# Kernel optimization log

Hardware: AMD Instinct MI355X
Metric: run time of the kernel (lower is better)

Reference implementation:

```python
import jax, jax.numpy as jnp
import numpy as np

N, K = 16384, 16          # nodes, neighbors per node
IN, HID, OUT = 256, 512, 512
HEADS, A = 8, 64          # heads * attention_size = 512
EPS = 1e-5


def _layernorm(x, g, b):
    m = x.mean(-1, keepdims=True)
    v = x.var(-1, keepdims=True)
    return (x - m) / jnp.sqrt(v + EPS) * g + b


def setup_inputs() -> dict:
    key = jax.random.key(0)
    ks = jax.random.split(key, 16)
    def lin(k, i, o):
        kw, kb = jax.random.split(k)
        w = jax.random.normal(kw, (i, o), jnp.float32) / np.sqrt(i).astype(np.float32)
        b = jax.random.normal(kb, (o,), jnp.float32) * 0.01
        return w, b
    inp = {}
    inp["data"] = jax.random.normal(ks[0], (N, IN), jnp.float32)
    inp["neighbors"] = jax.random.randint(ks[1], (N, K), 0, N, jnp.int32)
    inp["mlp_w0"], inp["mlp_b0"] = lin(ks[2], IN, HID)
    inp["mlp_w1"], inp["mlp_b1"] = lin(ks[3], HID, HID)
    inp["mlp_w2"], inp["mlp_b2"] = lin(ks[4], HID, HID)
    inp["pd_w"], inp["pd_b"] = lin(ks[5], IN, HID)   # project_down
    inp["pi_w"], inp["pi_b"] = lin(ks[6], IN, OUT)   # project_in
    inp["q_w"], inp["q_b"] = lin(ks[7], HID, HEADS * A)
    inp["k_w"], inp["k_b"] = lin(ks[8], HID, HEADS * A)
    inp["v_w"], inp["v_b"] = lin(ks[9], HID, HEADS * A)
    inp["o_w"], inp["o_b"] = lin(ks[10], HEADS * A, OUT)
    inp["ln1_g"] = jnp.ones((HID,), jnp.float32)
    inp["ln1_b"] = jnp.zeros((HID,), jnp.float32)
    inp["ln2_g"] = jnp.ones((OUT,), jnp.float32)
    inp["ln2_b"] = jnp.zeros((OUT,), jnp.float32)
    return inp


def reference(data, neighbors, mlp_w0, mlp_b0, mlp_w1, mlp_b1, mlp_w2, mlp_b2,
              pd_w, pd_b, pi_w, pi_b, q_w, q_b, k_w, k_b, v_w, v_b, o_w, o_b,
              ln1_g, ln1_b, ln2_g, ln2_b):
    # --- local MLP branch (3-layer MLP, elu between layers) ---
    h = jax.nn.elu(data @ mlp_w0 + mlp_b0)
    h = jax.nn.elu(h @ mlp_w1 + mlp_b1)
    h = h @ mlp_w2 + mlp_b2
    pd = data @ pd_w + pd_b                 # project_down(data), reused twice
    local = h + pd                          # MLP(data) + project_down(data)
    # dropout is identity in eval mode
    local = jax.nn.elu(_layernorm(local + pd, ln1_g, ln1_b))
    # --- neighbour dot multi-head attention ---
    q = (local @ q_w + q_b).reshape(N, HEADS, A)
    kk = (local @ k_w + k_b)
    vv = (local @ v_w + v_b)
    kn = kk[neighbors].reshape(N, K, HEADS, A)   # irregular gather
    vn = vv[neighbors].reshape(N, K, HEADS, A)
    scores = jnp.einsum('nha,nkha->nhk', q, kn) / np.float32(np.sqrt(A))
    w = jax.nn.softmax(scores, axis=-1)
    attn = jnp.einsum('nhk,nkha->nha', w, vn).reshape(N, HEADS * A)
    interaction = attn @ o_w + o_b
    # --- residual + output norm ---
    return _layernorm(interaction + data @ pi_w + pi_b, ln2_g, ln2_b)
```

## Files before the change

### kernel.cpp

```cpp
#include <hip/hip_runtime.h>
#include <hip/hip_fp8.h>

typedef _Float16 h16;
typedef _Float16 h16x8 __attribute__((ext_vector_type(8)));
typedef _Float16 h16x4 __attribute__((ext_vector_type(4)));
typedef _Float16 h16x2 __attribute__((ext_vector_type(2)));
typedef float f32x4 __attribute__((ext_vector_type(4)));

#define DEV static __device__ __forceinline__

static constexpr size_t OFF_DATA = 0;
static constexpr size_t OFF_W0T  = 4194304;
static constexpr size_t OFF_W1T  = 4325376;
static constexpr size_t OFF_W2PD = 4587520;
static constexpr size_t OFF_QKVT = 4980736;
static constexpr size_t OFF_OPIT = 5767168;
static constexpr size_t OFF_X1   = 6160384;
static constexpr size_t OFF_X2   = 14548992;
static constexpr size_t OFF_P    = 22937600;

DEV void gload16(const void* g, void* l)
{
    __builtin_amdgcn_global_load_lds(
        (__attribute__((address_space(1))) void*)(void*)g,
        (__attribute__((address_space(3))) void*)l, 16, 0, 0);
}

DEV float eluf(float x) { return x > 0.f ? x : __expf(x) - 1.f; }

DEV float f8tof(unsigned char b)
{
    __hip_fp8_e4m3 t; t.__x = (__hip_fp8_storage_t)b; return (float)t;
}

__global__ __launch_bounds__(256)
void k_cvt_data(const float* __restrict__ src, h16* __restrict__ dst)
{
    size_t i = ((size_t)blockIdx.x * 256 + threadIdx.x) * 4;
    float4 v = *(const float4*)(src + i);
    h16x4 o;
    o[0] = (h16)v.x; o[1] = (h16)v.y; o[2] = (h16)v.z; o[3] = (h16)v.w;
    *(h16x4*)(dst + i) = o;
}

__global__ void k_prep_w(const float* __restrict__ w0, const float* __restrict__ w1,
                         const float* __restrict__ w2, const float* __restrict__ pdw,
                         const float* __restrict__ qw, const float* __restrict__ kw,
                         const float* __restrict__ vw, const float* __restrict__ ow,
                         const float* __restrict__ piw, h16* __restrict__ ws)
{
    int b = blockIdx.x;
    const float* src; h16* dst; int K, dstStride, dstKOff = 0, tb; float scale = 1.f;
    const int N = 512;
    if (b < 128)       { src = w0;  dst = ws + OFF_W0T;           K = 256; dstStride = 256; tb = 0; }
    else if (b < 384)  { src = w1;  dst = ws + OFF_W1T;           K = 512; dstStride = 512; tb = 128; }
    else if (b < 640)  { src = w2;  dst = ws + OFF_W2PD;          K = 512; dstStride = 768; tb = 384; }
    else if (b < 768)  { src = pdw; dst = ws + OFF_W2PD;          K = 256; dstStride = 768; dstKOff = 512; scale = 2.f; tb = 640; }
    else if (b < 1024) { src = qw;  dst = ws + OFF_QKVT;          K = 512; dstStride = 512; tb = 768; }
    else if (b < 1280) { src = kw;  dst = ws + OFF_QKVT + 262144; K = 512; dstStride = 512; tb = 1024; }
    else if (b < 1536) { src = vw;  dst = ws + OFF_QKVT + 524288; K = 512; dstStride = 512; tb = 1280; }
    else if (b < 1792) { src = ow;  dst = ws + OFF_OPIT;          K = 512; dstStride = 768; tb = 1536; }
    else               { src = piw; dst = ws + OFF_OPIT;          K = 256; dstStride = 768; dstKOff = 512; tb = 1792; }
    int t = b - tb;
    int tilesK = K >> 5;
    int tk = t % tilesK, tn = t / tilesK;
    __shared__ float tile[32][33];
    int tx = threadIdx.x, ty = threadIdx.y;
    #pragma unroll
    for (int r = 0; r < 32; r += 8)
        tile[ty + r][tx] = src[(size_t)(tk * 32 + ty + r) * N + tn * 32 + tx] * scale;
    __syncthreads();
    #pragma unroll
    for (int r = 0; r < 32; r += 8) {
        int n = tn * 32 + ty + r, k = tk * 32 + tx;
        dst[(size_t)n * dstStride + dstKOff + k] = (h16)tile[tx][ty + r];
    }
}

template<int BIASMODE, bool DOELU, int NT>
__global__ __launch_bounds__(512, 4)
void k_gemm(const h16* __restrict__ A1, const h16* __restrict__ A2,
            const int K1, const int K2,
            const h16* __restrict__ BT,
            const float* __restrict__ bias1, const float* __restrict__ bias2,
            const float* __restrict__ bias3, const float b2scale,
            h16* __restrict__ out, unsigned char* __restrict__ out2, const int N)
{
    const int Kt = K1 + K2;
    __shared__ __align__(16) h16 sA[128 * 32];
    __shared__ __align__(16) h16 sB[128 * 32];
    const int tid  = threadIdx.x;
    const int lane = tid & 63;
    const int bswz = blockIdx.x;
    const int slot = bswz & 7;
    const int gg   = bswz >> 3;
    const int mBase = ((gg / NT) * 8 + slot) * 128;
    const int nBase = (gg % NT) * 128;
    const int w  = tid >> 6;
    const int wm = (w >> 2) * 64;
    const int wn = (w & 3) * 32;
    const f32x4 zero = {0.f, 0.f, 0.f, 0.f};
    f32x4 acc[4][2];
    #pragma unroll
    for (int i = 0; i < 4; ++i) {
        #pragma unroll
        for (int j = 0; j < 2; ++j) acc[i][j] = zero;
    }

    const int ldR = tid >> 2;
    const int ldC = (tid & 3) * 8;
    const int lm = lane & 15, lk = (lane >> 4) * 8;

    for (int k0 = 0; k0 < Kt; k0 += 32) {
        const h16* Ab; int Ak, As;
        if (k0 < K1) { Ab = A1; Ak = k0;      As = K1; }
        else         { Ab = A2; Ak = k0 - K1; As = K2; }
        gload16(Ab + (size_t)(mBase + ldR) * As + Ak + ldC, &sA[ldR * 32 + ldC]);
        gload16(BT + (size_t)(nBase + ldR) * Kt + k0 + ldC, &sB[ldR * 32 + ldC]);
        __syncthreads();
        h16x8 af[4], bfr[2];
        #pragma unroll
        for (int i = 0; i < 4; ++i) af[i]  = *(const h16x8*)&sA[(wm + i * 16 + lm) * 32 + lk];
        #pragma unroll
        for (int j = 0; j < 2; ++j) bfr[j] = *(const h16x8*)&sB[(wn + j * 16 + lm) * 32 + lk];
        #pragma unroll
        for (int i = 0; i < 4; ++i) {
            #pragma unroll
            for (int j = 0; j < 2; ++j)
                acc[i][j] = __builtin_amdgcn_mfma_f32_16x16x32_f16(af[i], bfr[j], acc[i][j], 0, 0, 0);
        }
        __syncthreads();
    }

    const int lr4 = (lane >> 4) * 4;
    #pragma unroll
    for (int j = 0; j < 2; ++j) {
        const int col = nBase + wn + j * 16 + lm;
        float bv;
        if (BIASMODE == 0) bv = bias1[col];
        else if (BIASMODE == 1) bv = bias1[col] + b2scale * bias2[col];
        else {
            const int seg = col >> 9;
            const float* bp = seg == 0 ? bias1 : (seg == 1 ? bias2 : bias3);
            bv = bp[col & 511];
        }
        #pragma unroll
        for (int i = 0; i < 4; ++i) {
            const int row0 = mBase + wm + i * 16 + lr4;
            #pragma unroll
            for (int r = 0; r < 4; ++r) {
                float v = acc[i][j][r] + bv;
                if (DOELU) v = eluf(v);
                if (BIASMODE == 2) {
                    if (col < 512) {
                        out[(size_t)(row0 + r) * 512 + col] = (h16)v;
                    } else {
                        __hip_fp8_e4m3 f8(v);
                        out2[(size_t)(row0 + r) * 1024 + (col - 512)] = (unsigned char)f8.__x;
                    }
                } else {
                    out[(size_t)(row0 + r) * N + col] = (h16)v;
                }
            }
        }
    }
}

template<bool DOELU, bool OUTF32>
__global__ __launch_bounds__(256)
void k_ln(const h16* __restrict__ X, const float* __restrict__ g, const float* __restrict__ b,
          h16* __restrict__ outH, float* __restrict__ outF)
{
    const int row  = blockIdx.x * 4 + (threadIdx.x >> 6);
    const int lane = threadIdx.x & 63;
    const h16x8 xv = *(const h16x8*)(X + (size_t)row * 512 + lane * 8);
    float v[8], s = 0.f, ss = 0.f;
    #pragma unroll
    for (int k = 0; k < 8; ++k) { v[k] = (float)xv[k]; s += v[k]; ss += v[k] * v[k]; }
    #pragma unroll
    for (int m = 1; m < 64; m <<= 1) { s += __shfl_xor(s, m, 64); ss += __shfl_xor(ss, m, 64); }
    const float mean = s * (1.f / 512.f);
    const float var  = ss * (1.f / 512.f) - mean * mean;
    const float rstd = rsqrtf(var + 1e-5f);
    #pragma unroll
    for (int k = 0; k < 8; ++k) {
        const int c = lane * 8 + k;
        float y = (v[k] - mean) * rstd * g[c] + b[c];
        if (DOELU) y = eluf(y);
        if (OUTF32) outF[(size_t)row * 512 + c] = y;
        else        outH[(size_t)row * 512 + c] = (h16)y;
    }
}

__global__ __launch_bounds__(64)
void k_attn(const h16* __restrict__ Q, const unsigned char* __restrict__ KV,
            const int* __restrict__ nbr, h16* __restrict__ outA)
{
    __shared__ __align__(16) unsigned char sKV[16 * 1024];
    const int n = blockIdx.x;
    const int lane = threadIdx.x;

    #pragma unroll
    for (int j = 0; j < 16; ++j) {
        const int idx = nbr[n * 16 + j];
        gload16(KV + (size_t)idx * 1024 + lane * 16, &sKV[j * 1024 + lane * 16]);
    }
    const h16x8 qv = *(const h16x8*)&Q[(size_t)n * 512 + lane * 8];

    asm volatile("s_waitcnt vmcnt(0)" ::: "memory");

    float qf[8];
    #pragma unroll
    for (int e = 0; e < 8; ++e) qf[e] = (float)qv[e];

    float s[16];
    #pragma unroll
    for (int j = 0; j < 16; ++j) {
        union { uint2 u; unsigned char b[8]; } U;
        U.u = *(const uint2*)&sKV[j * 1024 + lane * 8];
        float d = 0.f;
        #pragma unroll
        for (int e = 0; e < 8; ++e) d += qf[e] * f8tof(U.b[e]);
        s[j] = d;
    }
    #pragma unroll
    for (int m = 1; m < 8; m <<= 1) {
        #pragma unroll
        for (int j = 0; j < 16; ++j) s[j] += __shfl_xor(s[j], m, 64);
    }
    float mx = -1e30f;
    #pragma unroll
    for (int j = 0; j < 16; ++j) { s[j] *= 0.125f; mx = fmaxf(mx, s[j]); }
    float sum = 0.f;
    #pragma unroll
    for (int j = 0; j < 16; ++j) { s[j] = __expf(s[j] - mx); sum += s[j]; }
    const float rinv = 1.f / sum;

    float acc[8];
    #pragma unroll
    for (int e = 0; e < 8; ++e) acc[e] = 0.f;
    #pragma unroll
    for (int j = 0; j < 16; ++j) {
        const float w = s[j] * rinv;
        union { uint2 u; unsigned char b[8]; } U;
        U.u = *(const uint2*)&sKV[j * 1024 + 512 + lane * 8];
        #pragma unroll
        for (int e = 0; e < 8; ++e) acc[e] += w * f8tof(U.b[e]);
    }
    h16x8 o;
    #pragma unroll
    for (int e = 0; e < 8; ++e) o[e] = (h16)acc[e];
    *(h16x8*)&outA[(size_t)n * 512 + lane * 8] = o;
}

extern "C" void kernel_launch(void* const* d_in, const int* in_sizes, int n_in,
                              void* d_out, int out_size, void* d_ws, size_t ws_size,
                              hipStream_t stream)
{
    const float* data = (const float*)d_in[0];
    const int*   nbr  = (const int*)d_in[1];
    const float* w0   = (const float*)d_in[2];
    const float* b0   = (const float*)d_in[3];
    const float* w1   = (const float*)d_in[4];
    const float* b1   = (const float*)d_in[5];
    const float* w2   = (const float*)d_in[6];
    const float* b2   = (const float*)d_in[7];
    const float* pdw  = (const float*)d_in[8];
    const float* pdb  = (const float*)d_in[9];
    const float* piw  = (const float*)d_in[10];
    const float* pib  = (const float*)d_in[11];
    const float* qw   = (const float*)d_in[12];
    const float* qb   = (const float*)d_in[13];
    const float* kw   = (const float*)d_in[14];
    const float* kb   = (const float*)d_in[15];
    const float* vw   = (const float*)d_in[16];
    const float* vb   = (const float*)d_in[17];
    const float* ow   = (const float*)d_in[18];
    const float* ob   = (const float*)d_in[19];
    const float* ln1g = (const float*)d_in[20];
    const float* ln1b = (const float*)d_in[21];
    const float* ln2g = (const float*)d_in[22];
    const float* ln2b = (const float*)d_in[23];
    h16*   ws  = (h16*)d_ws;
    float* out = (float*)d_out;
    h16*   qbuf = (h16*)d_out;
    unsigned char* kv8 = (unsigned char*)(ws + OFF_X1);

    k_cvt_data<<<4096, 256, 0, stream>>>(data, ws + OFF_DATA);
    k_prep_w<<<1920, dim3(32, 8), 0, stream>>>(w0, w1, w2, pdw, qw, kw, vw, ow, piw, ws);

    k_gemm<0, true , 4><<<512, 512, 0, stream>>>(ws + OFF_DATA, nullptr, 256, 0, ws + OFF_W0T,
                                             b0, nullptr, nullptr, 0.f,
                                             ws + OFF_X1, nullptr, 512);
    k_gemm<0, true , 4><<<512, 512, 0, stream>>>(ws + OFF_X1, nullptr, 512, 0, ws + OFF_W1T,
                                             b1, nullptr, nullptr, 0.f,
                                             ws + OFF_X2, nullptr, 512);
    k_gemm<1, false, 4><<<512, 512, 0, stream>>>(ws + OFF_X2, ws + OFF_DATA, 512, 256, ws + OFF_W2PD,
                                             b2, pdb, nullptr, 2.f,
                                             ws + OFF_P, nullptr, 512);
    k_ln<true, false><<<4096, 256, 0, stream>>>(ws + OFF_P, ln1g, ln1b, ws + OFF_P, nullptr);
    k_gemm<2, false, 12><<<1536, 512, 0, stream>>>(ws + OFF_P, nullptr, 512, 0, ws + OFF_QKVT,
                                             qb, kb, vb, 0.f,
                                             qbuf, kv8, 1536);
    k_attn<<<16384, 64, 0, stream>>>(qbuf, kv8, nbr, ws + OFF_P);
    k_gemm<1, false, 4><<<512, 512, 0, stream>>>(ws + OFF_P, ws + OFF_DATA, 512, 256, ws + OFF_OPIT,
                                             ob, pib, nullptr, 1.f,
                                             ws + OFF_X1, nullptr, 512);
    k_ln<false, true><<<4096, 256, 0, stream>>>(ws + OFF_X1, ln2g, ln2b, nullptr, out);
}
```

Before: 285.0 us.

## Keep full-K weight slab resident in LDS and stream A directly from global

The GEMM is rewritten so each block loads an entire 64-column by K weight slab into LDS once, using an XOR-swizzled layout prepared by the weight-prep kernel. A fragments are then read straight from global memory with no per-K-step barriers, and each block computes a 256x64 tile with a 4x4 MFMA tile per wave. The concatenated-K GEMMs (W2+PD, O+PI) are split into two launches, where the second accumulates into the fp16 output through a read-modify-write. This removes the per-step __syncthreads and A staging, at the cost of more global A traffic, an extra launch, and fp16 rounding of the intermediate sum.

```diff
diff --git a/kernel.cpp b/kernel.cpp
--- a/kernel.cpp
+++ b/kernel.cpp
@@ -4,20 +4,21 @@
 typedef _Float16 h16;
 typedef _Float16 h16x8 __attribute__((ext_vector_type(8)));
 typedef _Float16 h16x4 __attribute__((ext_vector_type(4)));
-typedef _Float16 h16x2 __attribute__((ext_vector_type(2)));
 typedef float f32x4 __attribute__((ext_vector_type(4)));
 
 #define DEV static __device__ __forceinline__
 
-static constexpr size_t OFF_DATA = 0;
-static constexpr size_t OFF_W0T  = 4194304;
-static constexpr size_t OFF_W1T  = 4325376;
-static constexpr size_t OFF_W2PD = 4587520;
-static constexpr size_t OFF_QKVT = 4980736;
-static constexpr size_t OFF_OPIT = 5767168;
-static constexpr size_t OFF_X1   = 6160384;
-static constexpr size_t OFF_X2   = 14548992;
-static constexpr size_t OFF_P    = 22937600;
+static constexpr size_t OFF_DATA  = 0;
+static constexpr size_t SLAB_W0   = 4194304;
+static constexpr size_t SLAB_W1   = 4325376;
+static constexpr size_t SLAB_W2   = 4587520;
+static constexpr size_t SLAB_PD   = 4849664;
+static constexpr size_t SLAB_QKV  = 4980736;
+static constexpr size_t SLAB_OW   = 5767168;
+static constexpr size_t SLAB_PI   = 6029312;
+static constexpr size_t OFF_X1    = 6160384;
+static constexpr size_t OFF_X2    = 14548992;
+static constexpr size_t OFF_P     = 22937600;
 
 DEV void gload16(const void* g, void* l)
 {
@@ -49,117 +50,118 @@
                          const float* __restrict__ vw, const float* __restrict__ ow,
                          const float* __restrict__ piw, h16* __restrict__ ws)
 {
-    int b = blockIdx.x;
-    const float* src; h16* dst; int K, dstStride, dstKOff = 0, tb; float scale = 1.f;
-    const int N = 512;
-    if (b < 128)       { src = w0;  dst = ws + OFF_W0T;           K = 256; dstStride = 256; tb = 0; }
-    else if (b < 384)  { src = w1;  dst = ws + OFF_W1T;           K = 512; dstStride = 512; tb = 128; }
-    else if (b < 640)  { src = w2;  dst = ws + OFF_W2PD;          K = 512; dstStride = 768; tb = 384; }
-    else if (b < 768)  { src = pdw; dst = ws + OFF_W2PD;          K = 256; dstStride = 768; dstKOff = 512; scale = 2.f; tb = 640; }
-    else if (b < 1024) { src = qw;  dst = ws + OFF_QKVT;          K = 512; dstStride = 512; tb = 768; }
-    else if (b < 1280) { src = kw;  dst = ws + OFF_QKVT + 262144; K = 512; dstStride = 512; tb = 1024; }
-    else if (b < 1536) { src = vw;  dst = ws + OFF_QKVT + 524288; K = 512; dstStride = 512; tb = 1280; }
-    else if (b < 1792) { src = ow;  dst = ws + OFF_OPIT;          K = 512; dstStride = 768; tb = 1536; }
-    else               { src = piw; dst = ws + OFF_OPIT;          K = 256; dstStride = 768; dstKOff = 512; tb = 1792; }
-    int t = b - tb;
-    int tilesK = K >> 5;
-    int tk = t % tilesK, tn = t / tilesK;
-    __shared__ float tile[32][33];
-    int tx = threadIdx.x, ty = threadIdx.y;
-    #pragma unroll
-    for (int r = 0; r < 32; r += 8)
-        tile[ty + r][tx] = src[(size_t)(tk * 32 + ty + r) * N + tn * 32 + tx] * scale;
+    const int b = blockIdx.x;
+    const float* src; size_t dstBase; int K, tb; float scale = 1.f;
+    if (b < 32)       { src = w0;  dstBase = SLAB_W0;           K = 256; tb = 0; }
+    else if (b < 96)  { src = w1;  dstBase = SLAB_W1;           K = 512; tb = 32; }
+    else if (b < 160) { src = w2;  dstBase = SLAB_W2;           K = 512; tb = 96; }
+    else if (b < 192) { src = pdw; dstBase = SLAB_PD;           K = 256; scale = 2.f; tb = 160; }
+    else if (b < 256) { src = qw;  dstBase = SLAB_QKV;          K = 512; tb = 192; }
+    else if (b < 320) { src = kw;  dstBase = SLAB_QKV + 262144; K = 512; tb = 256; }
+    else if (b < 384) { src = vw;  dstBase = SLAB_QKV + 524288; K = 512; tb = 320; }
+    else if (b < 448) { src = ow;  dstBase = SLAB_OW;           K = 512; tb = 384; }
+    else              { src = piw; dstBase = SLAB_PI;           K = 256; tb = 448; }
+    const int t = b - tb;
+    const int ktiles = K >> 6;
+    const int kt = t % ktiles, nt = t / ktiles;
+    __shared__ float tile[64][65];
+    const int tid = threadIdx.x;
+    #pragma unroll
+    for (int r = 0; r < 16; ++r) {
+        const int idx = r * 256 + tid;
+        const int kk = idx >> 6, nn = idx & 63;
+        tile[kk][nn] = src[(size_t)(kt * 64 + kk) * 512 + nt * 64 + nn] * scale;
+    }
     __syncthreads();
     #pragma unroll
-    for (int r = 0; r < 32; r += 8) {
-        int n = tn * 32 + ty + r, k = tk * 32 + tx;
-        dst[(size_t)n * dstStride + dstKOff + k] = (h16)tile[tx][ty + r];
-    }
-}
-
-template<int BIASMODE, bool DOELU, int NT>
-__global__ __launch_bounds__(512, 4)
-void k_gemm(const h16* __restrict__ A1, const h16* __restrict__ A2,
-            const int K1, const int K2,
-            const h16* __restrict__ BT,
+    for (int r = 0; r < 2; ++r) {
+        const int ch = r * 256 + tid;
+        const int nl = ch >> 3, cl = ch & 7;
+        const int c  = kt * 8 + cl;
+        const int p  = c ^ (nl & 7);
+        h16x8 o;
+        #pragma unroll
+        for (int e = 0; e < 8; ++e) o[e] = (h16)tile[cl * 8 + e][nl];
+        *(h16x8*)&ws[dstBase + (size_t)nt * 64 * K + (size_t)nl * K + p * 8] = o;
+    }
+}
+
+template<int K, int BIASMODE, bool DOELU, bool ACC>
+__global__ __launch_bounds__(256, 2)
+void k_gemm(const h16* __restrict__ A, const h16* __restrict__ slab,
             const float* __restrict__ bias1, const float* __restrict__ bias2,
-            const float* __restrict__ bias3, const float b2scale,
-            h16* __restrict__ out, unsigned char* __restrict__ out2, const int N)
-{
-    const int Kt = K1 + K2;
-    __shared__ __align__(16) h16 sA[128 * 32];
-    __shared__ __align__(16) h16 sB[128 * 32];
-    const int tid  = threadIdx.x;
-    const int lane = tid & 63;
-    const int bswz = blockIdx.x;
-    const int slot = bswz & 7;
-    const int gg   = bswz >> 3;
-    const int mBase = ((gg / NT) * 8 + slot) * 128;
-    const int nBase = (gg % NT) * 128;
-    const int w  = tid >> 6;
-    const int wm = (w >> 2) * 64;
-    const int wn = (w & 3) * 32;
+            const float* __restrict__ bias3, const float s,
+            h16* __restrict__ out, unsigned char* __restrict__ out2)
+{
+    __shared__ __align__(16) h16 sB[64 * K];
+    const int tid = threadIdx.x, lane = tid & 63, w = tid >> 6;
+    const int mg = blockIdx.x & 63, ns = blockIdx.x >> 6;
+
+    const char* g = (const char*)(slab + (size_t)ns * 64 * K);
+    #pragma unroll
+    for (int r = 0; r < K / 32; ++r)
+        gload16(g + r * 4096 + tid * 16, (char*)sB + r * 4096 + tid * 16);
+    __syncthreads();
+
+    const int lm = lane & 15, lq = lane >> 4;
+    const int mBase = mg * 256 + w * 64;
     const f32x4 zero = {0.f, 0.f, 0.f, 0.f};
-    f32x4 acc[4][2];
+    f32x4 acc[4][4];
     #pragma unroll
     for (int i = 0; i < 4; ++i) {
         #pragma unroll
-        for (int j = 0; j < 2; ++j) acc[i][j] = zero;
-    }
-
-    const int ldR = tid >> 2;
-    const int ldC = (tid & 3) * 8;
-    const int lm = lane & 15, lk = (lane >> 4) * 8;
-
-    for (int k0 = 0; k0 < Kt; k0 += 32) {
-        const h16* Ab; int Ak, As;
-        if (k0 < K1) { Ab = A1; Ak = k0;      As = K1; }
-        else         { Ab = A2; Ak = k0 - K1; As = K2; }
-        gload16(Ab + (size_t)(mBase + ldR) * As + Ak + ldC, &sA[ldR * 32 + ldC]);
-        gload16(BT + (size_t)(nBase + ldR) * Kt + k0 + ldC, &sB[ldR * 32 + ldC]);
-        __syncthreads();
-        h16x8 af[4], bfr[2];
-        #pragma unroll
-        for (int i = 0; i < 4; ++i) af[i]  = *(const h16x8*)&sA[(wm + i * 16 + lm) * 32 + lk];
-        #pragma unroll
-        for (int j = 0; j < 2; ++j) bfr[j] = *(const h16x8*)&sB[(wn + j * 16 + lm) * 32 + lk];
+        for (int j = 0; j < 4; ++j) acc[i][j] = zero;
+    }
+
+    #pragma unroll 4
+    for (int ks = 0; ks < K / 32; ++ks) {
+        h16x8 a[4], bf[4];
+        #pragma unroll
+        for (int i = 0; i < 4; ++i)
+            a[i] = *(const h16x8*)&A[(size_t)(mBase + i * 16 + lm) * K + ks * 32 + lq * 8];
+        #pragma unroll
+        for (int j = 0; j < 4; ++j) {
+            const int nl = j * 16 + lm;
+            const int c  = ks * 4 + lq;
+            bf[j] = *(const h16x8*)&sB[nl * K + ((c ^ (lm & 7)) << 3)];
+        }
         #pragma unroll
         for (int i = 0; i < 4; ++i) {
             #pragma unroll
-            for (int j = 0; j < 2; ++j)
-                acc[i][j] = __builtin_amdgcn_mfma_f32_16x16x32_f16(af[i], bfr[j], acc[i][j], 0, 0, 0);
+            for (int j = 0; j < 4; ++j)
+                acc[i][j] = __builtin_amdgcn_mfma_f32_16x16x32_f16(a[i], bf[j], acc[i][j], 0, 0, 0);
         }
-        __syncthreads();
-    }
-
-    const int lr4 = (lane >> 4) * 4;
-    #pragma unroll
-    for (int j = 0; j < 2; ++j) {
-        const int col = nBase + wn + j * 16 + lm;
-        float bv;
+    }
+
+    const int lr4 = lq * 4;
+    #pragma unroll
+    for (int j = 0; j < 4; ++j) {
+        const int col = ns * 64 + j * 16 + lm;
+        float bv = 0.f;
         if (BIASMODE == 0) bv = bias1[col];
-        else if (BIASMODE == 1) bv = bias1[col] + b2scale * bias2[col];
-        else {
-            const int seg = col >> 9;
-            const float* bp = seg == 0 ? bias1 : (seg == 1 ? bias2 : bias3);
+        else if (BIASMODE == 1) bv = bias1[col] + s * bias2[col];
+        else if (BIASMODE == 2) {
+            const float* bp = ns < 8 ? bias1 : (ns < 16 ? bias2 : bias3);
             bv = bp[col & 511];
         }
         #pragma unroll
         for (int i = 0; i < 4; ++i) {
-            const int row0 = mBase + wm + i * 16 + lr4;
+            const int row0 = mBase + i * 16 + lr4;
             #pragma unroll
             for (int r = 0; r < 4; ++r) {
                 float v = acc[i][j][r] + bv;
                 if (DOELU) v = eluf(v);
                 if (BIASMODE == 2) {
-                    if (col < 512) {
+                    if (ns < 8) {
                         out[(size_t)(row0 + r) * 512 + col] = (h16)v;
                     } else {
                         __hip_fp8_e4m3 f8(v);
                         out2[(size_t)(row0 + r) * 1024 + (col - 512)] = (unsigned char)f8.__x;
                     }
                 } else {
-                    out[(size_t)(row0 + r) * N + col] = (h16)v;
+                    const size_t o = (size_t)(row0 + r) * 512 + col;
+                    if (ACC) v += (float)out[o];
+                    out[o] = (h16)v;
                 }
             }
         }
@@ -287,24 +289,30 @@
     unsigned char* kv8 = (unsigned char*)(ws + OFF_X1);
 
     k_cvt_data<<<4096, 256, 0, stream>>>(data, ws + OFF_DATA);
-    k_prep_w<<<1920, dim3(32, 8), 0, stream>>>(w0, w1, w2, pdw, qw, kw, vw, ow, piw, ws);
-
-    k_gemm<0, true , 4><<<512, 512, 0, stream>>>(ws + OFF_DATA, nullptr, 256, 0, ws + OFF_W0T,
-                                             b0, nullptr, nullptr, 0.f,
-                                             ws + OFF_X1, nullptr, 512);
-    k_gemm<0, true , 4><<<512, 512, 0, stream>>>(ws + OFF_X1, nullptr, 512, 0, ws + OFF_W1T,
-                                             b1, nullptr, nullptr, 0.f,
-                                             ws + OFF_X2, nullptr, 512);
-    k_gemm<1, false, 4><<<512, 512, 0, stream>>>(ws + OFF_X2, ws + OFF_DATA, 512, 256, ws + OFF_W2PD,
-                                             b2, pdb, nullptr, 2.f,
-                                             ws + OFF_P, nullptr, 512);
+    k_prep_w<<<480, 256, 0, stream>>>(w0, w1, w2, pdw, qw, kw, vw, ow, piw, ws);
+
+    k_gemm<256, 0, true , false><<<512, 256, 0, stream>>>(ws + OFF_DATA, ws + SLAB_W0,
+                                                          b0, nullptr, nullptr, 0.f,
+                                                          ws + OFF_X1, nullptr);
+    k_gemm<512, 0, true , false><<<512, 256, 0, stream>>>(ws + OFF_X1, ws + SLAB_W1,
+                                                          b1, nullptr, nullptr, 0.f,
+                                                          ws + OFF_X2, nullptr);
+    k_gemm<256, 1, false, false><<<512, 256, 0, stream>>>(ws + OFF_DATA, ws + SLAB_PD,
+                                                          b2, pdb, nullptr, 2.f,
+                                                          ws + OFF_P, nullptr);
+    k_gemm<512, 3, false, true ><<<512, 256, 0, stream>>>(ws + OFF_X2, ws + SLAB_W2,
+                                                          nullptr, nullptr, nullptr, 0.f,
+                                                          ws + OFF_P, nullptr);
     k_ln<true, false><<<4096, 256, 0, stream>>>(ws + OFF_P, ln1g, ln1b, ws + OFF_P, nullptr);
-    k_gemm<2, false, 12><<<1536, 512, 0, stream>>>(ws + OFF_P, nullptr, 512, 0, ws + OFF_QKVT,
-                                             qb, kb, vb, 0.f,
-                                             qbuf, kv8, 1536);
+    k_gemm<512, 2, false, false><<<1536, 256, 0, stream>>>(ws + OFF_P, ws + SLAB_QKV,
+                                                           qb, kb, vb, 0.f,
+                                                           qbuf, kv8);
     k_attn<<<16384, 64, 0, stream>>>(qbuf, kv8, nbr, ws + OFF_P);
-    k_gemm<1, false, 4><<<512, 512, 0, stream>>>(ws + OFF_P, ws + OFF_DATA, 512, 256, ws + OFF_OPIT,
-                                             ob, pib, nullptr, 1.f,
-                                             ws + OFF_X1, nullptr, 512);
-    k_ln<false, true><<<4096, 256, 0, stream>>>(ws + OFF_X1, ln2g, ln2b, nullptr, out);
-}
+    k_gemm<256, 1, false, false><<<512, 256, 0, stream>>>(ws + OFF_DATA, ws + SLAB_PI,
+                                                          ob, pib, nullptr, 1.f,
+                                                          ws + OFF_X2, nullptr);
+    k_gemm<512, 3, false, true ><<<512, 256, 0, stream>>>(ws + OFF_P, ws + SLAB_OW,
+                                                          nullptr, nullptr, nullptr, 0.f,
+                                                          ws + OFF_X2, nullptr);
+    k_ln<false, true><<<4096, 256, 0, stream>>>(ws + OFF_X2, ln2g, ln2b, nullptr, out);
+}
```

Result: slower. 354.7 us (+24.4%).
